# Performance work log

Hardware: AMD Instinct MI355X
Metric: run time of the kernel (lower is better)

Reference implementation:

```python
import jax, jax.numpy as jnp
import numpy as np
from jax import lax

NUM_HEADS = 4
DIM = 192
EPS = 1e-12  # torch F.normalize eps


def setup_inputs() -> dict:
    key = jax.random.key(0)
    ks = jax.random.split(key, 5)
    b, c, h, w = 8, DIM, 128, 128
    x = jax.random.normal(ks[0], (b, c, h, w), dtype=jnp.float32)
    f = jax.random.normal(ks[1], (b, c, h, w), dtype=jnp.float32)
    # conv weights, scaled like kaiming-ish init
    w_qkv = jax.random.normal(ks[2], (3 * c, c, 1, 1), dtype=jnp.float32) * (1.0 / np.sqrt(c))
    w_dw = jax.random.normal(ks[3], (3 * c, 1, 3, 3), dtype=jnp.float32) * (1.0 / 3.0)
    w_proj = jax.random.normal(ks[4], (c, c, 1, 1), dtype=jnp.float32) * (1.0 / np.sqrt(c))
    temperature = jnp.ones((NUM_HEADS, 1, 1), dtype=jnp.float32)
    return {"x": x, "f": f, "w_qkv": w_qkv, "w_dw": w_dw, "w_proj": w_proj,
            "temperature": temperature}


def _conv(x, w, groups=1):
    return lax.conv_general_dilated(
        x, w, window_strides=(1, 1), padding="SAME",
        dimension_numbers=("NCHW", "OIHW", "NCHW"),
        feature_group_count=groups)


def reference(x, f, w_qkv, w_dw, w_proj, temperature):
    b, c, h, w = x.shape
    x_in = x + f
    qkv = _conv(x_in, w_qkv)                 # [b, 3c, h, w] 1x1 conv
    qkv = _conv(qkv, w_dw, groups=3 * c)     # depthwise 3x3
    q, k, v = jnp.split(qkv, 3, axis=1)      # each [b, c, h, w]
    hw = h * w
    ch = c // NUM_HEADS

    def heads(t):
        return t.reshape(b, NUM_HEADS, ch, hw)  # 'b (head c) h w -> b head c (h w)'

    q, k, v = heads(q), heads(k), heads(v)
    # L2-normalize over spatial (last) dim, torch-style eps clamp
    q = q / jnp.maximum(jnp.linalg.norm(q, axis=-1, keepdims=True), EPS)
    k = k / jnp.maximum(jnp.linalg.norm(k, axis=-1, keepdims=True), EPS)
    # transposed (channel) attention: [b, head, ch, ch]
    attn = jnp.einsum("bhcn,bhdn->bhcd", q, k) * temperature[None]
    attn = jax.nn.softmax(attn, axis=-1)
    out = jnp.einsum("bhcd,bhdn->bhcn", attn, v)  # [b, head, ch, hw]
    out = out.reshape(b, c, h, w)
    return _conv(out, w_proj)
```

## Files before the change

### kernel.cpp

```cpp
#include <hip/hip_runtime.h>
#include <stdint.h>

#define NB 8
#define NC 192
#define NOC 576
#define NH 4
#define HW 16384
#define NCHUNK 16

typedef unsigned short u16;
typedef __bf16 v8bf __attribute__((ext_vector_type(8)));
typedef float v4f __attribute__((ext_vector_type(4)));
typedef u16 v8us __attribute__((ext_vector_type(8)));
typedef u16 v4us __attribute__((ext_vector_type(4)));

__device__ __forceinline__ u16 f2bf(float f) {
    uint32_t u = __float_as_uint(f);
    u += 0x7FFFu + ((u >> 16) & 1u);
    return (u16)(u >> 16);
}
__device__ __forceinline__ float bf2f(u16 u) {
    return __uint_as_float(((uint32_t)u) << 16);
}

__global__ void k_cvt_w(const float* __restrict__ w, u16* __restrict__ wb, int n) {
    int i = blockIdx.x * 256 + threadIdx.x;
    if (i < n) wb[i] = f2bf(w[i]);
}

__global__ __launch_bounds__(512, 4) void k_gemm_qkv(
    const float* __restrict__ x, const float* __restrict__ f,
    const u16* __restrict__ wb, u16* __restrict__ qkv, int b0)
{
    __shared__ u16 bt[64 * 192];
    __shared__ u16 wt[576 * 32];
    const int t = threadIdx.x;
    const int bl = blockIdx.y;
    const int bg = b0 + bl;
    const int p0 = blockIdx.x * 64;

    {
        const int px = t & 63;
        const int cg = t >> 6;
        #pragma unroll
        for (int it = 0; it < 3; ++it) {
            const int c4 = it * 8 + cg;
            const size_t base = ((size_t)bg * NC + c4 * 8) * HW + p0 + px;
            v8us pk;
            #pragma unroll
            for (int j = 0; j < 8; ++j) {
                float v = x[base + (size_t)j * HW] + f[base + (size_t)j * HW];
                pk[j] = f2bf(v);
            }
            *reinterpret_cast<v8us*>(&bt[px * 192 + ((c4 ^ (px & 7)) << 3)]) = pk;
        }
    }

    const int w = t >> 6, l = t & 63, lr = l & 15, lg = l >> 4;
    const int wp = w >> 2;
    const int wo = w & 3;
    const int oc0 = wo * 144;

    v4f acc[2][9];
    #pragma unroll
    for (int mi = 0; mi < 2; ++mi)
        #pragma unroll
        for (int ni = 0; ni < 9; ++ni)
            acc[mi][ni] = (v4f){0.f, 0.f, 0.f, 0.f};

    v8us wload[5];
    #pragma unroll
    for (int it = 0; it < 5; ++it) {
        const int idx = it * 512 + t;
        if (idx < 2304) {
            const int oc = idx >> 2, q = idx & 3;
            wload[it] = *reinterpret_cast<const v8us*>(&wb[oc * 192 + q * 8]);
        }
    }

    #pragma unroll 1
    for (int ks = 0; ks < 6; ++ks) {
        __syncthreads();
        #pragma unroll
        for (int it = 0; it < 5; ++it) {
            const int idx = it * 512 + t;
            if (idx < 2304) {
                const int oc = idx >> 2, q = idx & 3;
                const int g = (oc ^ (oc >> 2)) & 3;
                *reinterpret_cast<v8us*>(&wt[oc * 32 + ((q ^ g) << 3)]) = wload[it];
            }
        }
        if (ks < 5) {
            #pragma unroll
            for (int it = 0; it < 5; ++it) {
                const int idx = it * 512 + t;
                if (idx < 2304) {
                    const int oc = idx >> 2, q = idx & 3;
                    wload[it] = *reinterpret_cast<const v8us*>(&wb[oc * 192 + (ks + 1) * 32 + q * 8]);
                }
            }
        }
        __syncthreads();

        v8bf a[2];
        #pragma unroll
        for (int mi = 0; mi < 2; ++mi) {
            const int px = wp * 32 + mi * 16 + lr;
            a[mi] = *reinterpret_cast<const v8bf*>(&bt[px * 192 + (((ks * 4 + lg) ^ (px & 7)) << 3)]);
        }
        #pragma unroll
        for (int ni = 0; ni < 9; ++ni) {
            const int oc = oc0 + ni * 16 + lr;
            const int g = (oc ^ (oc >> 2)) & 3;
            const v8bf bw = *reinterpret_cast<const v8bf*>(&wt[oc * 32 + ((lg ^ g) << 3)]);
            #pragma unroll
            for (int mi = 0; mi < 2; ++mi)
                acc[mi][ni] = __builtin_amdgcn_mfma_f32_16x16x32_bf16(a[mi], bw, acc[mi][ni], 0, 0, 0);
        }
    }

    #pragma unroll
    for (int pass = 0; pass < 2; ++pass) {
        __syncthreads();
        if (wp == pass) {
            #pragma unroll
            for (int mi = 0; mi < 2; ++mi) {
                #pragma unroll
                for (int ni = 0; ni < 9; ++ni) {
                    const int oc = oc0 + ni * 16 + lr;
                    const int chunk = mi * 4 + lg;
                    const int sch = chunk ^ (oc & 7);
                    v4us pk;
                    pk[0] = f2bf(acc[mi][ni][0]); pk[1] = f2bf(acc[mi][ni][1]);
                    pk[2] = f2bf(acc[mi][ni][2]); pk[3] = f2bf(acc[mi][ni][3]);
                    *reinterpret_cast<v4us*>(&wt[oc * 32 + sch * 4]) = pk;
                }
            }
        }
        __syncthreads();
        #pragma unroll
        for (int rd = 0; rd < 9; ++rd) {
            const int idx = rd * 512 + t;
            const int oc = idx >> 3;
            const int c = idx & 7;
            v4us v = *reinterpret_cast<v4us*>(&wt[oc * 32 + (c ^ (oc & 7)) * 4]);
            *reinterpret_cast<v4us*>(&qkv[((size_t)bl * NOC + oc) * HW + p0 + pass * 32 + c * 4]) = v;
        }
    }
}

__global__ __launch_bounds__(256) void k_dw(
    const u16* __restrict__ qkv, const float* __restrict__ wdw,
    u16* __restrict__ qk_out, u16* __restrict__ v_out,
    float* __restrict__ sumsq, int b0)
{
    __shared__ u16 plane[128 * 136];
    __shared__ float red[4];
    const int t = threadIdx.x;
    const int ch = blockIdx.x;
    const int bl = blockIdx.y;
    const int bg = b0 + bl;
    const size_t pbase = ((size_t)bl * NOC + ch) * HW;

    float wk[9];
    #pragma unroll
    for (int i = 0; i < 9; ++i) wk[i] = wdw[ch * 9 + i];

    const int r = t >> 1;
    const int cb = (t & 1) * 64;

    #pragma unroll
    for (int i = 0; i < 8; ++i) {
        v8us v = *reinterpret_cast<const v8us*>(&qkv[pbase + r * 128 + cb + i * 8]);
        *reinterpret_cast<v8us*>(&plane[r * 136 + cb + i * 8]) = v;
    }
    __syncthreads();

    const bool vm = (r > 0), vp = (r < 127);
    const u16* rowm = &plane[(r - 1) * 136];
    const u16* rowc = &plane[r * 136];
    const u16* rowp = &plane[(r + 1) * 136];

    float am, ac, bm, bc, cm, cc2;
    if (cb == 0) { am = 0.f; bm = 0.f; cm = 0.f; }
    else {
        am = vm ? bf2f(rowm[cb - 1]) : 0.f;
        bm = bf2f(rowc[cb - 1]);
        cm = vp ? bf2f(rowp[cb - 1]) : 0.f;
    }
    ac = vm ? bf2f(rowm[cb]) : 0.f;
    bc = bf2f(rowc[cb]);
    cc2 = vp ? bf2f(rowp[cb]) : 0.f;

    uint32_t ov[32];
    float ssq = 0.f;
    #pragma unroll
    for (int xp = 0; xp < 32; ++xp) {
        #pragma unroll
        for (int s2 = 0; s2 < 2; ++s2) {
            const int col = cb + xp * 2 + s2;
            float ap, bp, cp;
            if (col < 127) {
                ap = vm ? bf2f(rowm[col + 1]) : 0.f;
                bp = bf2f(rowc[col + 1]);
                cp = vp ? bf2f(rowp[col + 1]) : 0.f;
            } else { ap = 0.f; bp = 0.f; cp = 0.f; }
            float o = wk[0]*am + wk[1]*ac + wk[2]*ap
                    + wk[3]*bm + wk[4]*bc + wk[5]*bp
                    + wk[6]*cm + wk[7]*cc2 + wk[8]*cp;
            u16 ob = f2bf(o);
            float orr = bf2f(ob);
            ssq += orr * orr;
            ov[xp] = (s2 == 0) ? (uint32_t)ob : (ov[xp] | ((uint32_t)ob << 16));
            am = ac; ac = ap; bm = bc; bc = bp; cm = cc2; cc2 = cp;
        }
    }

    __syncthreads();
    #pragma unroll
    for (int i = 0; i < 32; ++i)
        *reinterpret_cast<uint32_t*>(&plane[r * 136 + cb + i * 2]) = ov[i];
    __syncthreads();

    u16* dst = (ch < 2 * NC) ? (qk_out + ((size_t)bg * (2 * NC) + ch) * HW)
                             : (v_out + ((size_t)bg * NC + (ch - 2 * NC)) * HW);
    #pragma unroll
    for (int i = 0; i < 8; ++i) {
        const int idx = i * 2048 + t * 8;
        const int rr = idx >> 7, cc = idx & 127;
        v8us v = *reinterpret_cast<const v8us*>(&plane[rr * 136 + cc]);
        *reinterpret_cast<v8us*>(&dst[idx]) = v;
    }

    #pragma unroll
    for (int off = 32; off > 0; off >>= 1) ssq += __shfl_down(ssq, off);
    if ((t & 63) == 0) red[t >> 6] = ssq;
    __syncthreads();
    if (t == 0 && ch < 2 * NC) sumsq[bg * (2 * NC) + ch] = red[0] + red[1] + red[2] + red[3];
}

__global__ __launch_bounds__(256) void k_attn(
    const u16* __restrict__ qk, float* __restrict__ partials)
{
    __shared__ float wsum[4 * 2304];
    const int t = threadIdx.x;
    const int chunk = blockIdx.x;
    const int h = blockIdx.y;
    const int b = blockIdx.z;
    const int w = t >> 6, l = t & 63, lr = l & 15, lg = l >> 4;

    const size_t qbase = ((size_t)b * 384 + h * 48) * HW;
    const size_t kbase = ((size_t)b * 384 + 192 + h * 48) * HW;
    const int pb = chunk * 1024 + w * 256;

    v4f acc[3][3];
    #pragma unroll
    for (int mi = 0; mi < 3; ++mi)
        #pragma unroll
        for (int ni = 0; ni < 3; ++ni)
            acc[mi][ni] = (v4f){0.f, 0.f, 0.f, 0.f};

    #pragma unroll
    for (int ks = 0; ks < 8; ++ks) {
        const int k = pb + ks * 32 + lg * 8;
        v8bf a[3], bb[3];
        #pragma unroll
        for (int mi = 0; mi < 3; ++mi)
            a[mi] = *reinterpret_cast<const v8bf*>(&qk[qbase + (size_t)(mi * 16 + lr) * HW + k]);
        #pragma unroll
        for (int ni = 0; ni < 3; ++ni)
            bb[ni] = *reinterpret_cast<const v8bf*>(&qk[kbase + (size_t)(ni * 16 + lr) * HW + k]);
        #pragma unroll
        for (int mi = 0; mi < 3; ++mi)
            #pragma unroll
            for (int ni = 0; ni < 3; ++ni)
                acc[mi][ni] = __builtin_amdgcn_mfma_f32_16x16x32_bf16(a[mi], bb[ni], acc[mi][ni], 0, 0, 0);
    }

    #pragma unroll
    for (int mi = 0; mi < 3; ++mi)
        #pragma unroll
        for (int ni = 0; ni < 3; ++ni)
            #pragma unroll
            for (int r = 0; r < 4; ++r)
                wsum[w * 2304 + (mi * 16 + lg * 4 + r) * 48 + ni * 16 + lr] = acc[mi][ni][r];
    __syncthreads();

    #pragma unroll
    for (int i = 0; i < 9; ++i) {
        const int e = t + i * 256;
        float s = wsum[e] + wsum[2304 + e] + wsum[4608 + e] + wsum[6912 + e];
        partials[(((size_t)(b * NH + h)) * NCHUNK + chunk) * 2304 + e] = s;
    }
}

__global__ __launch_bounds__(256) void k_smx(
    const float* __restrict__ partials, const float* __restrict__ sumsq,
    const float* __restrict__ wproj, const float* __restrict__ temp,
    u16* __restrict__ Mb)
{
    __shared__ float att[2304];
    __shared__ float rq[48], rk[48];
    const int t = threadIdx.x;
    const int h = blockIdx.x;
    const int b = blockIdx.y;

    if (t < 48) {
        float s = sumsq[b * 384 + h * 48 + t];
        rq[t] = 1.f / fmaxf(sqrtf(s), 1e-12f);
    } else if (t < 96) {
        float s = sumsq[b * 384 + 192 + h * 48 + (t - 48)];
        rk[t - 48] = 1.f / fmaxf(sqrtf(s), 1e-12f);
    }
    __syncthreads();
    const float tp = temp[h];
    #pragma unroll
    for (int i = 0; i < 9; ++i) {
        const int e = t + i * 256;
        const float* pp = &partials[(((size_t)(b * NH + h)) * NCHUNK) * 2304 + e];
        float s = 0.f;
        #pragma unroll
        for (int c = 0; c < NCHUNK; ++c) s += pp[(size_t)c * 2304];
        att[e] = s * rq[e / 48] * rk[e % 48] * tp;
    }
    __syncthreads();
    if (t < 48) {
        float m = -1e30f;
        #pragma unroll
        for (int j = 0; j < 48; ++j) m = fmaxf(m, att[t * 48 + j]);
        float s = 0.f;
        for (int j = 0; j < 48; ++j) { float e2 = __expf(att[t * 48 + j] - m); att[t * 48 + j] = e2; s += e2; }
        const float inv = 1.f / s;
        for (int j = 0; j < 48; ++j) att[t * 48 + j] *= inv;
    }
    __syncthreads();
    #pragma unroll
    for (int i = 0; i < 36; ++i) {
        const int idx = t + i * 256;
        const int oc = idx / 48, d = idx % 48;
        float s = 0.f;
        #pragma unroll
        for (int cc = 0; cc < 48; ++cc)
            s += wproj[oc * 192 + h * 48 + cc] * att[cc * 48 + d];
        Mb[((size_t)b * NC + oc) * NC + h * 48 + d] = f2bf(s);
    }
}

__global__ __launch_bounds__(256) void k_gemm_out(
    const u16* __restrict__ vp, const u16* __restrict__ Mb,
    float* __restrict__ out)
{
    __shared__ u16 bt[64 * 192];
    const int t = threadIdx.x;
    const int b = blockIdx.y;
    const int p0 = blockIdx.x * 64;

    {
        const int px = t & 63;
        const int cg = t >> 6;
        #pragma unroll
        for (int it = 0; it < 6; ++it) {
            const int c4 = it * 4 + cg;
            const size_t base = ((size_t)b * NC + c4 * 8) * HW + p0 + px;
            v8us pk;
            #pragma unroll
            for (int j = 0; j < 8; ++j) pk[j] = vp[base + (size_t)j * HW];
            *reinterpret_cast<v8us*>(&bt[px * 192 + ((c4 ^ (px & 7)) << 3)]) = pk;
        }
    }
    __syncthreads();

    const int w = t >> 6, l = t & 63, lr = l & 15, lg = l >> 4;
    const int oc0 = w * 48;

    v4f acc[4][3];
    #pragma unroll
    for (int mi = 0; mi < 4; ++mi)
        #pragma unroll
        for (int ni = 0; ni < 3; ++ni)
            acc[mi][ni] = (v4f){0.f, 0.f, 0.f, 0.f};

    #pragma unroll
    for (int ks = 0; ks < 6; ++ks) {
        const int k = ks * 32 + lg * 8;
        const int c4 = ks * 4 + lg;
        v8bf a[4];
        #pragma unroll
        for (int mi = 0; mi < 4; ++mi) {
            const int px = mi * 16 + lr;
            a[mi] = *reinterpret_cast<const v8bf*>(&bt[px * 192 + ((c4 ^ (px & 7)) << 3)]);
        }
        #pragma unroll
        for (int ni = 0; ni < 3; ++ni) {
            const int oc = oc0 + ni * 16 + lr;
            const v8bf bw = *reinterpret_cast<const v8bf*>(&Mb[((size_t)b * NC + oc) * NC + k]);
            #pragma unroll
            for (int mi = 0; mi < 4; ++mi)
                acc[mi][ni] = __builtin_amdgcn_mfma_f32_16x16x32_bf16(a[mi], bw, acc[mi][ni], 0, 0, 0);
        }
    }

    #pragma unroll
    for (int mi = 0; mi < 4; ++mi)
        #pragma unroll
        for (int ni = 0; ni < 3; ++ni) {
            const int oc = oc0 + ni * 16 + lr;
            const int px = p0 + mi * 16 + lg * 4;
            *reinterpret_cast<v4f*>(&out[((size_t)b * NC + oc) * HW + px]) = acc[mi][ni];
        }
}

extern "C" void kernel_launch(void* const* d_in, const int* in_sizes, int n_in,
                              void* d_out, int out_size, void* d_ws, size_t ws_size,
                              hipStream_t stream)
{
    (void)in_sizes; (void)n_in; (void)out_size;
    const float* x      = (const float*)d_in[0];
    const float* f      = (const float*)d_in[1];
    const float* w_qkv  = (const float*)d_in[2];
    const float* w_dw   = (const float*)d_in[3];
    const float* w_proj = (const float*)d_in[4];
    const float* temp   = (const float*)d_in[5];

    char* ws = (char*)d_ws;
    u16*   vws      = (u16*)(ws);
    u16*   wb       = (u16*)(ws + 50331648);
    float* sumsq    = (float*)(ws + 50552832);
    float* partials = (float*)(ws + 50565120);
    u16*   Mb       = (u16*)(ws + 55283712);
    const size_t FIXED = 55873536;
    const size_t PERB  = (size_t)NOC * HW * 2;
    u16*   qkv_raw  = (u16*)(ws + FIXED);

    int g = 1;
    if (ws_size > FIXED + PERB) {
        size_t avail = (ws_size - FIXED) / PERB;
        g = (int)(avail > 8 ? 8 : avail);
        if (g < 1) g = 1;
    }

    u16* qk_scratch = (u16*)d_out;
    float* out      = (float*)d_out;

    hipLaunchKernelGGL(k_cvt_w, dim3(432), dim3(256), 0, stream, w_qkv, wb, NOC * NC);
    for (int b0 = 0; b0 < NB; b0 += g) {
        const int nb = (b0 + g <= NB) ? g : (NB - b0);
        hipLaunchKernelGGL(k_gemm_qkv, dim3(HW / 64, nb), dim3(512), 0, stream, x, f, wb, qkv_raw, b0);
        hipLaunchKernelGGL(k_dw, dim3(NOC, nb), dim3(256), 0, stream, qkv_raw, w_dw, qk_scratch, vws, sumsq, b0);
    }
    hipLaunchKernelGGL(k_attn, dim3(NCHUNK, NH, NB), dim3(256), 0, stream, qk_scratch, partials);
    hipLaunchKernelGGL(k_smx, dim3(NH, NB), dim3(256), 0, stream, partials, sumsq, w_proj, temp, Mb);
    hipLaunchKernelGGL(k_gemm_out, dim3(HW / 64, NB), dim3(256), 0, stream, vws, Mb, out);
}
```

Baseline: 301.7 us.

## Store QKV intermediate in pixel-block-major layout for contiguous GEMM epilogue writes

The QKV GEMM epilogue now writes its whole 576x64 output tile in one pass as a contiguous 72KB block, using a blocked layout of [batch][pixel-block][channel][64 pixels], instead of two half-tile passes of strided per-channel 64-byte rows. This removes one sync/store round and allows 16-byte vector global stores. The depthwise kernel's plane load is changed to gather 128-byte runs from 256 separate pixel blocks per channel. The write side becomes fully coalesced, but the read side becomes more scattered.

```diff
diff --git a/kernel.cpp b/kernel.cpp
--- a/kernel.cpp
+++ b/kernel.cpp
@@ -32,12 +32,14 @@
     const float* __restrict__ x, const float* __restrict__ f,
     const u16* __restrict__ wb, u16* __restrict__ qkv, int b0)
 {
-    __shared__ u16 bt[64 * 192];
-    __shared__ u16 wt[576 * 32];
+    __shared__ u16 smem[36864];
+    u16* bt = smem;
+    u16* wt = smem + 12288;
     const int t = threadIdx.x;
     const int bl = blockIdx.y;
     const int bg = b0 + bl;
-    const int p0 = blockIdx.x * 64;
+    const int pblk = blockIdx.x;
+    const int p0 = pblk * 64;
 
     {
         const int px = t & 63;
@@ -119,33 +121,35 @@
         }
     }
 
-    #pragma unroll
-    for (int pass = 0; pass < 2; ++pass) {
-        __syncthreads();
-        if (wp == pass) {
-            #pragma unroll
-            for (int mi = 0; mi < 2; ++mi) {
-                #pragma unroll
-                for (int ni = 0; ni < 9; ++ni) {
-                    const int oc = oc0 + ni * 16 + lr;
-                    const int chunk = mi * 4 + lg;
-                    const int sch = chunk ^ (oc & 7);
-                    v4us pk;
-                    pk[0] = f2bf(acc[mi][ni][0]); pk[1] = f2bf(acc[mi][ni][1]);
-                    pk[2] = f2bf(acc[mi][ni][2]); pk[3] = f2bf(acc[mi][ni][3]);
-                    *reinterpret_cast<v4us*>(&wt[oc * 32 + sch * 4]) = pk;
-                }
-            }
-        }
-        __syncthreads();
-        #pragma unroll
-        for (int rd = 0; rd < 9; ++rd) {
-            const int idx = rd * 512 + t;
-            const int oc = idx >> 3;
-            const int c = idx & 7;
-            v4us v = *reinterpret_cast<v4us*>(&wt[oc * 32 + (c ^ (oc & 7)) * 4]);
-            *reinterpret_cast<v4us*>(&qkv[((size_t)bl * NOC + oc) * HW + p0 + pass * 32 + c * 4]) = v;
-        }
+    __syncthreads();
+    u16* et = smem;
+    #pragma unroll
+    for (int mi = 0; mi < 2; ++mi)
+        #pragma unroll
+        for (int ni = 0; ni < 9; ++ni) {
+            const int oc = oc0 + ni * 16 + lr;
+            const int u = wp * 8 + mi * 4 + lg;
+            const int su = u ^ (oc & 15);
+            v4us pk;
+            pk[0] = f2bf(acc[mi][ni][0]); pk[1] = f2bf(acc[mi][ni][1]);
+            pk[2] = f2bf(acc[mi][ni][2]); pk[3] = f2bf(acc[mi][ni][3]);
+            *reinterpret_cast<v4us*>(&et[oc * 64 + su * 4]) = pk;
+        }
+    __syncthreads();
+    const size_t obase = ((size_t)bl * 256 + pblk) * 36864;
+    #pragma unroll
+    for (int rd = 0; rd < 9; ++rd) {
+        const int idx = rd * 512 + t;
+        const int oc = idx >> 3;
+        const int ck = idx & 7;
+        const int u0 = (ck * 2) ^ (oc & 15);
+        const int u1 = (ck * 2 + 1) ^ (oc & 15);
+        v4us lo = *reinterpret_cast<v4us*>(&et[oc * 64 + u0 * 4]);
+        v4us hi = *reinterpret_cast<v4us*>(&et[oc * 64 + u1 * 4]);
+        v8us o8;
+        o8[0] = lo[0]; o8[1] = lo[1]; o8[2] = lo[2]; o8[3] = lo[3];
+        o8[4] = hi[0]; o8[5] = hi[1]; o8[6] = hi[2]; o8[7] = hi[3];
+        *reinterpret_cast<v8us*>(&qkv[obase + (size_t)idx * 8]) = o8;
     }
 }
 
@@ -160,7 +164,6 @@
     const int ch = blockIdx.x;
     const int bl = blockIdx.y;
     const int bg = b0 + bl;
-    const size_t pbase = ((size_t)bl * NOC + ch) * HW;
 
     float wk[9];
     #pragma unroll
@@ -169,10 +172,16 @@
     const int r = t >> 1;
     const int cb = (t & 1) * 64;
 
-    #pragma unroll
-    for (int i = 0; i < 8; ++i) {
-        v8us v = *reinterpret_cast<const v8us*>(&qkv[pbase + r * 128 + cb + i * 8]);
-        *reinterpret_cast<v8us*>(&plane[r * 136 + cb + i * 8]) = v;
+    {
+        const u16* src = qkv + ((size_t)bl * 256) * 36864 + (size_t)ch * 64;
+        #pragma unroll
+        for (int i = 0; i < 8; ++i) {
+            const int e = i * 2048 + t * 8;
+            const int pblk = e >> 6, px = e & 63;
+            v8us v = *reinterpret_cast<const v8us*>(&src[(size_t)pblk * 36864 + px]);
+            const int rr = e >> 7, cc = e & 127;
+            *reinterpret_cast<v8us*>(&plane[rr * 136 + cc]) = v;
+        }
     }
     __syncthreads();
 
```

Result: faster. 295.2 us (-2.2%).
